# Kernel optimization log

Measured on AMD Instinct MI355X. Metric: run time of the kernel, lower is better.

The kernel has to match this reference:

```python
import jax, jax.numpy as jnp
import numpy as np

A = 3                      # anchors per location
HS = [256, 128, 64, 32]    # square feature-map sizes (FPN levels)
B = 4                      # batch (num images)
SIZES = [A * h * h for h in HS]
T = sum(SIZES)             # 261120 anchors per image
PRE_N, POST_N = 512, 512
NMS_TH, SCORE_TH, MIN_SIZE = 0.7, 0.0, 1e-3
LOG_MAX = 4.135166556742356   # log(1000/16), standard delta clamp
MAXV = 8                      # max vertices of quad-quad intersection
LVL_OFF = 8192.0              # per-level coordinate offset for batched NMS


def box_corners(b):
    # b: [..., 5] (cx, cy, w, h, angle) -> [..., 4, 2] CCW corners
    cx, cy, w, h, a = (b[..., i] for i in range(5))
    c, s = jnp.cos(a), jnp.sin(a)
    dx = 0.5 * jnp.stack([w, -w, -w, w], -1)
    dy = 0.5 * jnp.stack([h, h, -h, -h], -1)
    x = cx[..., None] + dx * c[..., None] - dy * s[..., None]
    y = cy[..., None] + dx * s[..., None] + dy * c[..., None]
    return jnp.stack([x, y], -1)


def _clip(poly, cnt, p1, p2):
    # Sutherland-Hodgman clip of poly (padded [MAXV,2], cnt valid) by half-plane left of p1->p2
    e = p2 - p1
    d = e[0] * (poly[:, 1] - p1[1]) - e[1] * (poly[:, 0] - p1[0])
    def body(carry, i):
        out, oc = carry
        nxt = jnp.where(i + 1 < cnt, i + 1, 0)
        cur_in, nxt_in = d[i] >= 0, d[nxt] >= 0
        valid = i < cnt
        keep = valid & cur_in
        out = out.at[oc].set(jnp.where(keep, poly[i], out[oc]))
        oc = oc + keep.astype(jnp.int32)
        crs = valid & (cur_in != nxt_in)
        den = d[i] - d[nxt]
        t = d[i] / jnp.where(den == 0, 1.0, den)
        ip = poly[i] + t * (poly[nxt] - poly[i])
        out = out.at[oc].set(jnp.where(crs, ip, out[oc]))
        oc = oc + crs.astype(jnp.int32)
        return (out, oc), None
    (out, oc), _ = jax.lax.scan(body, (jnp.zeros((MAXV, 2), poly.dtype), jnp.int32(0)), jnp.arange(MAXV))
    return out, oc


def _inter_area(ca, cb):
    # intersection area of two convex quads given CCW corners [4,2]
    poly = jnp.zeros((MAXV, 2), ca.dtype).at[:4].set(ca)
    cnt = jnp.int32(4)
    for k in range(4):
        poly, cnt = _clip(poly, cnt, cb[k], cb[(k + 1) % 4])
    i = jnp.arange(MAXV)
    nxt = jnp.where(i + 1 < cnt, i + 1, 0)
    cr = poly[i, 0] * poly[nxt, 1] - poly[nxt, 0] * poly[i, 1]
    area = 0.5 * jnp.abs(jnp.sum(jnp.where(i < cnt, cr, 0.0)))
    return jnp.where(cnt >= 3, area, 0.0)


def decode(deltas, anchors):
    # XYWHA decode with 6-dim deltas (dx,dy,dw,dh,dsin,dcos), weights all 1.0
    ax, ay, aw, ah, aa = (anchors[..., i] for i in range(5))
    dx, dy, dw, dh, ds, dc = (deltas[..., i] for i in range(6))
    dw = jnp.minimum(dw, LOG_MAX)
    dh = jnp.minimum(dh, LOG_MAX)
    return jnp.stack([ax + dx * aw, ay + dy * ah, aw * jnp.exp(dw),
                      ah * jnp.exp(dh), aa + jnp.arctan2(ds, dc)], -1)


def nms_image(boxes, scores, levels):
    # boxes [N,5], scores [N] (post-sigmoid), levels [N] int32 -> fixed-size padded outputs
    N = scores.shape[0]
    valid = (boxes[:, 2] >= MIN_SIZE) & (boxes[:, 3] >= MIN_SIZE) & (scores >= SCORE_TH)
    s = jnp.where(valid, scores, -jnp.inf)
    order = jnp.argsort(-s)
    bx, sc, vd = boxes[order], s[order], valid[order]
    off = levels[order].astype(bx.dtype) * LVL_OFF
    nb = bx.at[:, :2].add(off[:, None])          # level offset => cross-level IoU == 0
    nbg = jax.lax.stop_gradient(nb)
    corners = box_corners(nbg)                    # [N,4,2]
    areas = nbg[:, 2] * nbg[:, 3]
    CH = 128
    def chunk_fn(args):
        cc, ca = args
        def row(ci, ai):
            inter = jax.vmap(lambda cj: _inter_area(ci, cj))(corners)
            return inter / (ai + areas - inter + 1e-7)
        return jax.vmap(row)(cc, ca)
    iou = jax.lax.map(chunk_fn, (corners.reshape(N // CH, CH, 4, 2),
                                 areas.reshape(N // CH, CH))).reshape(N, N)
    idx = jnp.arange(N)
    def body(i, sup):
        keep_i = ~sup[i]
        return sup | (keep_i & (iou[i] > NMS_TH) & (idx > i))
    sup = jax.lax.fori_loop(0, N, body, ~vd)      # invalid boxes start suppressed
    kept = ~sup
    _, top_i = jax.lax.top_k(jnp.where(kept, sc, -jnp.inf), POST_N)
    ok = kept[top_i]
    return jnp.where(ok[:, None], bx[top_i], 0.0), jnp.where(ok, sc[top_i], 0.0)


def rpn_forward(objs, dlts, anchors):
    obj_f, dlt_f = [], []
    for o, d, h in zip(objs, dlts, HS):
        # permute_and_flatten: [B,A,H,W] -> [B,H*W*A]; [B,A*6,H,W] -> [B,H*W*A,6]
        obj_f.append(o.transpose(0, 2, 3, 1).reshape(B, -1))
        dlt_f.append(d.reshape(B, A, 6, h, h).transpose(0, 3, 4, 1, 2).reshape(B, -1, 6))
    objectness = jnp.concatenate(obj_f, 1)        # [B, T]
    deltas = jnp.concatenate(dlt_f, 1)            # [B, T, 6]
    proposals = decode(deltas, anchors)           # [B, T, 5]
    parts, offset = [], 0
    for sz in SIZES:                               # per-level top-k
        k = min(PRE_N, sz)
        _, ti = jax.lax.top_k(objectness[:, offset:offset + sz], k)
        parts.append(ti + offset)
        offset += sz
    top_idx = jnp.concatenate(parts, 1)           # [B, 4*PRE_N]
    levels = jnp.concatenate([jnp.full((sz,), i, jnp.int32) for i, sz in enumerate(SIZES)])
    obj_top = jnp.take_along_axis(objectness, top_idx, 1)
    prop_top = jnp.take_along_axis(proposals, top_idx[..., None], 1)
    lvl_top = levels[top_idx]
    scores = jax.nn.sigmoid(obj_top)
    return jax.vmap(nms_image)(prop_top, scores, lvl_top)


def setup_inputs() -> dict:
    key = jax.random.key(0)
    ks = jax.random.split(key, 9)
    inp = {}
    for i, h in enumerate(HS):
        inp[f"obj{i}"] = jax.random.normal(ks[i], (B, A, h, h), jnp.float32)
        inp[f"dlt{i}"] = 0.25 * jax.random.normal(ks[4 + i], (B, A * 6, h, h), jnp.float32)
    u = jax.random.uniform(ks[8], (B, T, 5), jnp.float32)
    inp["anchors"] = jnp.stack([u[..., 0] * 1024.0, u[..., 1] * 1024.0,
                                8.0 + 120.0 * u[..., 2], 8.0 + 120.0 * u[..., 3],
                                jnp.pi * (u[..., 4] - 0.5)], -1)
    return inp


def reference(obj0, obj1, obj2, obj3, dlt0, dlt1, dlt2, dlt3, anchors):
    # returns (boxes [B, POST_N, 5], scores [B, POST_N]) padded with zeros
    return rpn_forward([obj0, obj1, obj2, obj3], [dlt0, dlt1, dlt2, dlt3], anchors)
```

## Files before the change

kernel.cpp:

```cpp
#include <hip/hip_runtime.h>

typedef unsigned int u32;
typedef unsigned long long u64;
typedef unsigned char u8;

#define NB 4
#define T_ANCH 261120
#define NCAND 2048
#define KSEL 512
#define POSTN 512
#define LOG_MAXF 4.135166556742356f
#define NMS_TH 0.7f
#define LVL_OFF_F 8192.0f
#define BINS 4096
#define EQCAP 8192
#define K5_BLOCKS 2048
#define K1_BLOCKS 256

__device__ __forceinline__ u32 mono32(float f){
  u32 u = __float_as_uint(f);
  return (u & 0x80000000u) ? ~u : (u | 0x80000000u);
}
__device__ __forceinline__ int lvl_hw(int lvl){ return 65536 >> (2*lvl); }
__device__ __forceinline__ int lvl_off(int lvl){
  return (lvl>0?196608:0) + (lvl>1?49152:0) + (lvl>2?12288:0);
}
__device__ __forceinline__ void k1_map(int bx, int& b, int& lvl, int& ch){
  b = bx >> 6;
  int c = bx & 63;
  if (c < 48){ lvl = 0; ch = c; }
  else if (c < 60){ lvl = 1; ch = c - 48; }
  else if (c < 63){ lvl = 2; ch = c - 60; }
  else { lvl = 3; ch = 0; }
}

__global__ __launch_bounds__(1024) void k1_hist_thresh(
    const float* __restrict__ o0, const float* __restrict__ o1,
    const float* __restrict__ o2, const float* __restrict__ o3,
    u32* __restrict__ hist16, u32* __restrict__ done16,
    u32* __restrict__ gb0, u32* __restrict__ gcA)
{
  int b, lvl, ch;
  k1_map(blockIdx.x, b, lvl, ch);
  int bid16 = b*4 + lvl;
  int nch = (lvl==0?48 : lvl==1?12 : lvl==2?3 : 1);
  const float* ob = (lvl==0)?o0 : (lvl==1)?o1 : (lvl==2)?o2 : o3;
  int hw = lvl_hw(lvl);
  int size = 3*hw;
  int n4 = size >> 2;
  int i4 = ch*1024 + threadIdx.x;
  __shared__ u32 hist[BINS];
  __shared__ u32 coarse[64];
  __shared__ int s_last;
  for (int i = threadIdx.x; i < BINS; i += 1024) hist[i] = 0;
  __syncthreads();
  if (i4 < n4){
    float4 v = ((const float4*)(ob + (size_t)b*size))[i4];
    atomicAdd(&hist[mono32(v.x) >> 20], 1u);
    atomicAdd(&hist[mono32(v.y) >> 20], 1u);
    atomicAdd(&hist[mono32(v.z) >> 20], 1u);
    atomicAdd(&hist[mono32(v.w) >> 20], 1u);
  }
  __syncthreads();
  u32* gh = hist16 + (size_t)bid16*BINS;
  for (int i = threadIdx.x; i < BINS; i += 1024){
    u32 c = hist[i];
    if (c) atomicAdd(&gh[i], c);
  }
  __syncthreads();
  if (threadIdx.x == 0){
    __threadfence();
    u32 d = atomicAdd(&done16[bid16], 1u);
    s_last = (d == (u32)(nch - 1)) ? 1 : 0;
  }
  __syncthreads();
  if (!s_last) return;

  __threadfence();
  for (int i = threadIdx.x; i < BINS; i += 1024)
    hist[i] = __hip_atomic_load(&gh[i], __ATOMIC_RELAXED, __HIP_MEMORY_SCOPE_AGENT);
  __syncthreads();
  int t = threadIdx.x;
  if (t < 64){
    u32 s = 0;
    for (int z = 0; z < 64; ++z) s += hist[t*64 + z];
    coarse[t] = s;
  }
  __syncthreads();
  if (t == 0){
    u32 acc = 0;
    int cb = 63;
    while (acc + coarse[cb] < (u32)KSEL){ acc += coarse[cb]; --cb; }
    int z = cb*64 + 63;
    while (acc + hist[z] < (u32)KSEL){ acc += hist[z]; --z; }
    gb0[bid16] = (u32)z;
    gcA[bid16] = acc;
  }
}

__global__ __launch_bounds__(1024) void k2_classify(
    const float* __restrict__ o0, const float* __restrict__ o1,
    const float* __restrict__ o2, const float* __restrict__ o3,
    const u32* __restrict__ gb0,
    u32* __restrict__ emitcnt, u32* __restrict__ tiecnt,
    int* __restrict__ cand_j, u64* __restrict__ gtie)
{
  int b, lvl, ch;
  k1_map(blockIdx.x, b, lvl, ch);
  int bid16 = b*4 + lvl;
  const float* ob = (lvl==0)?o0 : (lvl==1)?o1 : (lvl==2)?o2 : o3;
  int hw = lvl_hw(lvl);
  int size = 3*hw;
  int n4 = size >> 2;
  int i4 = ch*1024 + threadIdx.x;

  __shared__ u32 dbuf[KSEL];
  __shared__ u64 tbuf[4096];
  __shared__ u32 dn, tn, dbase, tbase;
  if (threadIdx.x == 0){ dn = 0; tn = 0; }
  __syncthreads();

  u32 b0v = gb0[bid16];
  if (i4 < n4){
    float4 v = ((const float4*)(ob + (size_t)b*size))[i4];
    int L = i4 << 2;
    int a = L / hw;
    int pix = L - a*hw;
    int j0 = pix*3 + a;
    float vv[4] = {v.x, v.y, v.z, v.w};
    #pragma unroll
    for (int q = 0; q < 4; ++q){
      u32 m = mono32(vv[q]);
      u32 bin = m >> 20;
      int j = j0 + 3*q;
      if (bin > b0v){
        u32 s = atomicAdd(&dn, 1u);
        if (s < (u32)KSEL) dbuf[s] = (u32)j;
      } else if (bin == b0v){
        u32 s = atomicAdd(&tn, 1u);
        if (s < 4096u) tbuf[s] = ((u64)m << 32) | (u32)(~(u32)j);
      }
    }
  }
  __syncthreads();
  if (threadIdx.x == 0){
    dbase = dn ? atomicAdd(&emitcnt[bid16], dn) : 0u;
    tbase = tn ? atomicAdd(&tiecnt[bid16], tn) : 0u;
  }
  __syncthreads();
  for (u32 x = threadIdx.x; x < dn; x += 1024){
    u32 s = dbase + x;
    if (s < (u32)KSEL) cand_j[bid16*KSEL + s] = (int)dbuf[x];
  }
  for (u32 x = threadIdx.x; x < tn; x += 1024){
    u32 s = tbase + x;
    if (s < (u32)EQCAP) gtie[(size_t)bid16*EQCAP + s] = tbuf[x];
  }
}

__global__ __launch_bounds__(512) void k3_tie_decode(
    const u64* __restrict__ gtie, const u32* __restrict__ tiecnt,
    const u32* __restrict__ gcA, const int* __restrict__ cand_j,
    const float* __restrict__ o0, const float* __restrict__ o1,
    const float* __restrict__ o2, const float* __restrict__ o3,
    const float* __restrict__ d0, const float* __restrict__ d1,
    const float* __restrict__ d2, const float* __restrict__ d3,
    const float* __restrict__ anchors,
    float* __restrict__ cscore, u32* __restrict__ csmono,
    u64* __restrict__ ctb, float* __restrict__ cbox, u8* __restrict__ cvalid)
{
  int bid = blockIdx.x;
  int t = threadIdx.x;
  __shared__ u64 eq[EQCAP];
  __shared__ u32 wbuf[KSEL];
  __shared__ int jlist[KSEL];
  __shared__ u32 wn;
  u32 n = tiecnt[bid]; if (n > (u32)EQCAP) n = (u32)EQCAP;
  u32 cA = gcA[bid];
  u32 k = (u32)KSEL - cA;
  if (t == 0) wn = 0;
  for (int i = t; i < KSEL; i += 512) jlist[i] = 0;
  for (u32 i = t; i < n; i += 512) eq[i] = gtie[(size_t)bid*EQCAP + i];
  __syncthreads();
  for (u32 i = t; i < n; i += 512){
    u64 ki = eq[i];
    u32 r = 0;
    for (u32 m = 0; m < n; ++m) r += (eq[m] > ki) ? 1u : 0u;
    if (r < k){
      u32 s = atomicAdd(&wn, 1u);
      if (s < (u32)KSEL) wbuf[s] = (u32)(~(u32)ki);
    }
  }
  __syncthreads();
  u32 w = wn;
  for (u32 i = t; i < cA; i += 512)
    if (i < (u32)KSEL) jlist[i] = cand_j[bid*KSEL + i];
  for (u32 x = t; x < w; x += 512){
    u32 s = cA + x;
    if (s < (u32)KSEL) jlist[s] = (int)wbuf[x];
  }
  __syncthreads();

  {
    int c = bid*KSEL + t;
    int b = bid >> 2, lvl = bid & 3;
    int j = jlist[t];
    int hw = lvl_hw(lvl);
    u32 pix = (u32)j / 3u;
    u32 a = (u32)j - pix*3u;
    const float* ob = (lvl==0)?o0 : (lvl==1)?o1 : (lvl==2)?o2 : o3;
    const float* dl = (lvl==0)?d0 : (lvl==1)?d1 : (lvl==2)?d2 : d3;

    float ov = ob[(size_t)(b*3 + (int)a)*hw + pix];
    size_t dbase = ((size_t)(b*3 + (int)a)*6)*(size_t)hw + pix;
    float dx  = dl[dbase + 0*(size_t)hw];
    float dy  = dl[dbase + 1*(size_t)hw];
    float dw  = dl[dbase + 2*(size_t)hw];
    float dh  = dl[dbase + 3*(size_t)hw];
    float dsn = dl[dbase + 4*(size_t)hw];
    float dcs = dl[dbase + 5*(size_t)hw];
    int tt = lvl_off(lvl) + j;
    const float* an = anchors + ((size_t)b*T_ANCH + tt)*5;
    float ax=an[0], ay=an[1], aw=an[2], ah=an[3], aa=an[4];
    dw = fminf(dw, LOG_MAXF); dh = fminf(dh, LOG_MAXF);
    float cx = ax + dx*aw;
    float cy = ay + dy*ah;
    float ww = aw * expf(dw);
    float hh = ah * expf(dh);
    float ang = aa + atan2f(dsn, dcs);
    double sd = 1.0 / (1.0 + exp(-(double)ov));
    float sc = (float)sd;
    bool valid = (ww >= 1e-3f) && (hh >= 1e-3f) && (sc >= 0.0f);
    cscore[c] = sc;
    csmono[c] = valid ? mono32(sc) : 0u;
    ctb[c] = ((u64)lvl << 50) | ((u64)(u32)(~mono32(ov)) << 18) | (u64)(u32)j;
    cvalid[c] = valid ? 1 : 0;
    float* bb = cbox + (size_t)c*5;
    bb[0]=cx; bb[1]=cy; bb[2]=ww; bb[3]=hh; bb[4]=ang;
  }
}

__global__ __launch_bounds__(256) void k4_rank(
    const u32* __restrict__ csmono, const u64* __restrict__ ctb,
    const float* __restrict__ cscore, const float* __restrict__ cbox,
    const u8* __restrict__ cvalid,
    float* __restrict__ sscore, float* __restrict__ sbox,
    float* __restrict__ geom, float4* __restrict__ aabb4,
    u8* __restrict__ svalid, u64* __restrict__ maskz, u64* __restrict__ rowflagz)
{
  int b   = blockIdx.x >> 6;
  int blk = blockIdx.x & 63;
  __shared__ u32 sm[NCAND];
  __shared__ u64 stb[NCAND];
  __shared__ u32 cnt[32][8];
  {
    u64* mz = maskz + (size_t)blockIdx.x * 1024;
    for (int x = threadIdx.x; x < 1024; x += 256) mz[x] = 0ull;
    if (threadIdx.x == 0 && blockIdx.x < NB*32) rowflagz[blockIdx.x] = 0ull;
  }
  for (int k = threadIdx.x; k < NCAND; k += 256){
    sm[k]  = csmono[b*NCAND + k];
    stb[k] = ctb[b*NCAND + k];
  }
  __syncthreads();
  int esub = threadIdx.x >> 3;
  int ssub = threadIdx.x & 7;
  int id = blk*32 + esub;
  u32 ms = sm[id];
  u64 mt = stb[id];
  u32 r = 0;
  #pragma unroll 8
  for (int it = 0; it < 256; ++it){
    int m = it*8 + ssub;
    u32 s2 = sm[m]; u64 t2 = stb[m];
    r += ((s2 > ms) || (s2 == ms && t2 < mt)) ? 1u : 0u;
  }
  cnt[esub][ssub] = r;
  __syncthreads();
  if (ssub == 0){
    u32 rank = 0;
    #pragma unroll
    for (int q = 0; q < 8; ++q) rank += cnt[esub][q];
    int gsrc = b*NCAND + id;
    int gdst = b*NCAND + (int)rank;
    sscore[gdst] = cscore[gsrc];
    svalid[gdst] = cvalid[gsrc];
    float b0 = cbox[(size_t)gsrc*5+0], b1 = cbox[(size_t)gsrc*5+1];
    float b2 = cbox[(size_t)gsrc*5+2], b3 = cbox[(size_t)gsrc*5+3];
    float b4 = cbox[(size_t)gsrc*5+4];
    float* sb = sbox + (size_t)gdst*5;
    sb[0]=b0; sb[1]=b1; sb[2]=b2; sb[3]=b3; sb[4]=b4;
    int lvl = (int)((mt >> 50) & 3ull);
    float offv = (float)lvl * LVL_OFF_F;
    float cx = b0 + offv, cy = b1 + offv, w=b2, h=b3, ang=b4;
    float cc = cosf(ang), sn = sinf(ang);
    float hx = 0.5f*w, hy = 0.5f*h;
    float x0 = cx + hx*cc - hy*sn, y0 = cy + hx*sn + hy*cc;
    float x1 = cx - hx*cc - hy*sn, y1 = cy - hx*sn + hy*cc;
    float x2 = cx - hx*cc + hy*sn, y2 = cy - hx*sn - hy*cc;
    float x3 = cx + hx*cc + hy*sn, y3 = cy + hx*sn - hy*cc;
    float minx = fminf(fminf(x0,x1),fminf(x2,x3));
    float maxx = fmaxf(fmaxf(x0,x1),fmaxf(x2,x3));
    float miny = fminf(fminf(y0,y1),fminf(y2,y3));
    float maxy = fmaxf(fmaxf(y0,y1),fmaxf(y2,y3));
    float* g = geom + (size_t)gdst*16;
    g[0]=minx; g[1]=maxx; g[2]=miny; g[3]=maxy; g[4]=w*h;
    g[5]=x0; g[6]=y0; g[7]=x1; g[8]=y1; g[9]=x2; g[10]=y2; g[11]=x3; g[12]=y3;
    aabb4[gdst] = make_float4(minx, maxx, miny, maxy);
  }
}

__device__ __forceinline__ void emit_pt(float* ox, float* oy, int oc, float x, float y){
  #pragma unroll
  for (int s = 0; s < 8; ++s) if (s == oc){ ox[s] = x; oy[s] = y; }
}

__device__ float quad_inter(const float* ca, const float* cb){
  float px[8], py[8];
  #pragma unroll
  for (int q = 0; q < 8; ++q){ px[q]=0.f; py[q]=0.f; }
  #pragma unroll
  for (int q = 0; q < 4; ++q){ px[q]=ca[2*q]; py[q]=ca[2*q+1]; }
  int cnt = 4;
  #pragma unroll
  for (int e = 0; e < 4; ++e){
    float p1x = cb[2*e],         p1y = cb[2*e+1];
    float p2x = cb[(2*e+2)&7],   p2y = cb[(2*e+3)&7];
    float ex = p2x-p1x, ey = p2y-p1y;
    float d[8];
    #pragma unroll
    for (int q = 0; q < 8; ++q) d[q] = ex*(py[q]-p1y) - ey*(px[q]-p1x);
    float ox[8], oy[8];
    #pragma unroll
    for (int q = 0; q < 8; ++q){ ox[q]=0.f; oy[q]=0.f; }
    int oc = 0;
    #pragma unroll
    for (int q = 0; q < 8; ++q){
      if (q < cnt){
        bool last = (q+1 >= cnt);
        float dn  = last ? d[0]  : d[(q+1)&7];
        bool in0 = (d[q] >= 0.0f), in1 = (dn >= 0.0f);
        if (in0){ emit_pt(ox,oy,oc,px[q],py[q]); oc++; }
        if (in0 != in1){
          float pnx = last ? px[0] : px[(q+1)&7];
          float pny = last ? py[0] : py[(q+1)&7];
          float den = d[q] - dn;
          float t = d[q] / ((den == 0.0f) ? 1.0f : den);
          emit_pt(ox,oy,oc, px[q] + t*(pnx-px[q]), py[q] + t*(pny-py[q]));
          oc++;
        }
      }
    }
    cnt = (oc > 8) ? 8 : oc;
    #pragma unroll
    for (int q = 0; q < 8; ++q){ px[q]=ox[q]; py[q]=oy[q]; }
  }
  if (cnt < 3) return 0.0f;
  float s = 0.0f;
  #pragma unroll
  for (int q = 0; q < 8; ++q){
    if (q < cnt){
      bool last = (q+1 >= cnt);
      float pnx = last ? px[0] : px[(q+1)&7];
      float pny = last ? py[0] : py[(q+1)&7];
      s += px[q]*pny - pnx*py[q];
    }
  }
  return 0.5f*fabsf(s);
}

__global__ __launch_bounds__(256) void k5_pairs(
    const float4* __restrict__ aabb4, const float* __restrict__ geom,
    u64* __restrict__ mask, u64* __restrict__ rowflag)
{
  __shared__ u32 lbuf[4096];
  __shared__ u32 lcnt;
  if (threadIdx.x == 0) lcnt = 0;
  __syncthreads();
  int img = blockIdx.x >> 9;
  int kk  = blockIdx.x & 511;
  int lane = threadIdx.x & 63;
  int rows[4] = {2*kk, 2*kk + 1, 2046 - 2*kk, 2047 - 2*kk};
  #pragma unroll
  for (int r = 0; r < 4; ++r){
    int i = rows[r];
    float4 gi = aabb4[img*NCAND + i];
    for (int j = i + 1 + (int)threadIdx.x; j < NCAND; j += 256){
      float4 gj = aabb4[img*NCAND + j];
      bool pass = !(gi.x > gj.y || gj.x > gi.y || gi.z > gj.w || gj.z > gi.w);
      u64 bm = __ballot(pass);
      if (bm){
        int leader = __ffsll((long long)bm) - 1;
        u32 base = 0;
        if (lane == leader) base = atomicAdd(&lcnt, (u32)__popcll(bm));
        base = (u32)__shfl((int)base, leader);
        if (pass){
          u32 off = (u32)__popcll(bm & ((1ull << lane) - 1ull));
          lbuf[base + off] = (u32)((i << 11) | j);
        }
      }
    }
  }
  __syncthreads();
  u32 n = lcnt;
  for (u32 x = threadIdx.x; x < n; x += 256){
    u32 gt = lbuf[x];
    int i = (int)(gt >> 11);
    int j = (int)(gt & (NCAND-1));
    const float* gi = geom + ((size_t)(img*NCAND + i))*16;
    const float* gj = geom + ((size_t)(img*NCAND + j))*16;
    float inter = quad_inter(gi+5, gj+5);
    float iou = inter / (gi[4] + gj[4] - inter + 1e-7f);
    if (iou > NMS_TH){
      atomicOr(&mask[((size_t)(img*NCAND + i))*32 + (j >> 6)], 1ull << (j & 63));
      atomicOr(&rowflag[(size_t)img*32 + (i >> 6)], 1ull << (i & 63));
    }
  }
}

__global__ __launch_bounds__(1024) void k6_nms_out(
    const u64* __restrict__ mask, const u64* __restrict__ rowflag,
    const u8* __restrict__ svalid,
    const float* __restrict__ sbox, const float* __restrict__ sscore,
    float* __restrict__ out)
{
  int b = blockIdx.x;
  __shared__ u32 fid[NCAND];
  __shared__ u32 wcnt[32], wpref[32];
  __shared__ u64 s_kept[32];
  __shared__ u32 pref[32];
  __shared__ u32 s_F;
  int t = threadIdx.x;
  int wid = t >> 6, lane = t & 63;

  if (t < 32) wcnt[t] = (u32)__popcll(rowflag[b*32 + t]);
  __syncthreads();
  if (t == 0){
    u32 run = 0;
    for (int w = 0; w < 32; ++w){ wpref[w] = run; run += wcnt[w]; }
    s_F = run;
  }
  __syncthreads();
  if (t < 32){
    u64 fw = rowflag[b*32 + t];
    u32 o = wpref[t];
    while (fw){
      int bpos = __builtin_ctzll(fw);
      fid[o++] = (u32)(t*64 + bpos);
      fw &= fw - 1;
    }
  }
  for (int x = t; x < POSTN*5; x += 1024) out[(size_t)b*POSTN*5 + x] = 0.0f;
  for (int x = t; x < POSTN;   x += 1024) out[(size_t)NB*POSTN*5 + b*POSTN + x] = 0.0f;
  __syncthreads();

  if (wid == 0){
    u32 slo = 0, shi = 0;
    {
      int wl = lane & 31;
      u64 w = 0;
      for (int q = 0; q < 64; ++q)
        if (!svalid[b*NCAND + wl*64 + q]) w |= (1ull << q);
      slo = (u32)w; shi = (u32)(w >> 32);
    }
    u32 F = s_F;
    const u64* mb = mask + ((size_t)b*NCAND)*32;
    for (u32 f = 0; f < F; f += 8){
      u32 myfid = 0;
      if (f + (lane & 7) < F) myfid = fid[f + (lane & 7)];
      u64 v[8];
      #pragma unroll
      for (int q = 0; q < 8; ++q){
        if (f + q < F){
          u32 fq = (u32)__builtin_amdgcn_readlane((int)myfid, q);
          v[q] = mb[(size_t)fq*32 + (lane & 31)];
        } else v[q] = 0ull;
      }
      #pragma unroll
      for (int q = 0; q < 8; ++q){
        if (f + q < F){
          u32 i = (u32)__builtin_amdgcn_readlane((int)myfid, q);
          int wi = (int)(i >> 6);
          u32 wlo = (u32)__builtin_amdgcn_readlane((int)slo, wi);
          u32 whi = (u32)__builtin_amdgcn_readlane((int)shi, wi);
          u64 w = ((u64)whi << 32) | wlo;
          u32 keep = (u32)((~w >> (i & 63)) & 1ull);
          u64 vm = v[q] & (0ull - (u64)keep);
          slo |= (u32)vm; shi |= (u32)(vm >> 32);
        }
      }
    }
    if (lane < 32) s_kept[lane] = ~(((u64)shi << 32) | slo);
  }
  __syncthreads();

  if (t < 32) pref[t] = (u32)__popcll(s_kept[t]);
  __syncthreads();
  if (t == 0){
    u32 run = 0;
    for (int w = 0; w < 32; ++w){ u32 tv = pref[w]; pref[w] = run; run += tv; }
  }
  __syncthreads();
  for (int i = t; i < NCAND; i += 1024){
    u64 kw = s_kept[i >> 6];
    if ((kw >> (i & 63)) & 1ull){
      u32 rank = pref[i >> 6] + (u32)__popcll(kw & ((1ull << (i & 63)) - 1ull));
      if (rank < POSTN){
        const float* bp = sbox + ((size_t)(b*NCAND + i))*5;
        float* op = out + ((size_t)(b*POSTN + rank))*5;
        op[0]=bp[0]; op[1]=bp[1]; op[2]=bp[2]; op[3]=bp[3]; op[4]=bp[4];
        out[(size_t)NB*POSTN*5 + b*POSTN + rank] = sscore[b*NCAND + i];
      }
    }
  }
}

extern "C" void kernel_launch(void* const* d_in, const int* in_sizes, int n_in,
                              void* d_out, int out_size, void* d_ws, size_t ws_size,
                              hipStream_t stream)
{
  (void)out_size; (void)ws_size;
  const float *obj[4] = {nullptr,nullptr,nullptr,nullptr};
  const float *dlt[4] = {nullptr,nullptr,nullptr,nullptr};
  const float *anchors = nullptr;
  for (int i = 0; i < n_in; ++i){
    int s = in_sizes[i];
    const float* p = (const float*)d_in[i];
    switch (s){
      case 786432:  obj[0] = p; break;
      case 4718592: dlt[0] = p; break;
      case 196608:  obj[1] = p; break;
      case 1179648: dlt[1] = p; break;
      case 49152:   obj[2] = p; break;
      case 294912:  dlt[2] = p; break;
      case 12288:   obj[3] = p; break;
      case 73728:   dlt[3] = p; break;
      case 5222400: anchors = p; break;
      default: break;
    }
  }

  char* wsb = (char*)d_ws;
  size_t off = 0;
  auto alloc = [&](size_t bytes)->void*{
    size_t cur = (off + 255) & ~(size_t)255;
    off = cur + bytes;
    return (void*)(wsb + cur);
  };
  int*   cand_j = (int*)  alloc(16*KSEL*sizeof(int));
  float* cscore = (float*)alloc((size_t)NB*NCAND*sizeof(float));
  u32*   csmono = (u32*)  alloc((size_t)NB*NCAND*sizeof(u32));
  u64*   ctb    = (u64*)  alloc((size_t)NB*NCAND*sizeof(u64));
  float* cbox   = (float*)alloc((size_t)NB*NCAND*5*sizeof(float));
  u8*    cvalid = (u8*)   alloc((size_t)NB*NCAND);
  float* sscore = (float*)alloc((size_t)NB*NCAND*sizeof(float));
  float* sbox   = (float*)alloc((size_t)NB*NCAND*5*sizeof(float));
  u8*    svalid = (u8*)   alloc((size_t)NB*NCAND);
  float* geom   = (float*)alloc((size_t)NB*NCAND*16*sizeof(float));
  float4* aabb4 = (float4*)alloc((size_t)NB*NCAND*sizeof(float4));
  u64*   gtie   = (u64*)  alloc((size_t)16*EQCAP*sizeof(u64));
  u64*   maskp  = (u64*)  alloc((size_t)NB*NCAND*32*sizeof(u64));
  u64*   rowflag= (u64*)  alloc((size_t)NB*32*sizeof(u64));
  u32*   gb0    = (u32*)  alloc(16*sizeof(u32));
  u32*   gcA    = (u32*)  alloc(16*sizeof(u32));
  u32*   hist16 = (u32*)  alloc((size_t)16*BINS*sizeof(u32));
  u32*   done16 = (u32*)  alloc(16*sizeof(u32));
  u32*   emitc  = (u32*)  alloc(16*sizeof(u32));
  u32*   tiec   = (u32*)  alloc(16*sizeof(u32));
  size_t zero_len = (size_t)((wsb + off) - (char*)hist16);

  hipMemsetAsync(hist16, 0, zero_len, stream);

  hipLaunchKernelGGL(k1_hist_thresh, dim3(K1_BLOCKS), dim3(1024), 0, stream,
                     obj[0], obj[1], obj[2], obj[3], hist16, done16, gb0, gcA);
  hipLaunchKernelGGL(k2_classify, dim3(K1_BLOCKS), dim3(1024), 0, stream,
                     obj[0], obj[1], obj[2], obj[3], gb0, emitc, tiec,
                     cand_j, gtie);
  hipLaunchKernelGGL(k3_tie_decode, dim3(16), dim3(512), 0, stream,
                     gtie, tiec, gcA, cand_j,
                     obj[0], obj[1], obj[2], obj[3],
                     dlt[0], dlt[1], dlt[2], dlt[3],
                     anchors, cscore, csmono, ctb, cbox, cvalid);
  hipLaunchKernelGGL(k4_rank, dim3(256), dim3(256), 0, stream,
                     csmono, ctb, cscore, cbox, cvalid, sscore, sbox, geom,
                     aabb4, svalid, maskp, rowflag);
  hipLaunchKernelGGL(k5_pairs, dim3(K5_BLOCKS), dim3(256), 0, stream,
                     aabb4, geom, maskp, rowflag);
  hipLaunchKernelGGL(k6_nms_out, dim3(4), dim3(1024), 0, stream,
                     maskp, rowflag, svalid, sbox, sscore, (float*)d_out);
}
```

Measured before the change: 192.3 us.

## Fuse all RPN stages into one cooperative persistent kernel with grid syncs

Replaces the memset and six separate kernel launches with a single cooperative kernel of 256 blocks of 1024 threads. Stages are separated by grid-wide barriers, and a shared-memory union is reused across stages. Zeroing of the workspace and output is folded into the first stage. The aim is to remove launch gaps and the memset, but stages that used many smaller blocks (pair tests, ranking) now run on a fixed grid with grid-sync overhead, and the large shared union may limit occupancy.

```diff
diff --git a/kernel.cpp b/kernel.cpp
--- a/kernel.cpp
+++ b/kernel.cpp
@@ -1,4 +1,7 @@
 #include <hip/hip_runtime.h>
+#include <hip/hip_cooperative_groups.h>
+
+namespace cg = cooperative_groups;
 
 typedef unsigned int u32;
 typedef unsigned long long u64;
@@ -14,8 +17,7 @@
 #define LVL_OFF_F 8192.0f
 #define BINS 4096
 #define EQCAP 8192
-#define K5_BLOCKS 2048
-#define K1_BLOCKS 256
+#define GRID 256
 
 __device__ __forceinline__ u32 mono32(float f){
   u32 u = __float_as_uint(f);
@@ -32,282 +34,6 @@
   else if (c < 60){ lvl = 1; ch = c - 48; }
   else if (c < 63){ lvl = 2; ch = c - 60; }
   else { lvl = 3; ch = 0; }
-}
-
-__global__ __launch_bounds__(1024) void k1_hist_thresh(
-    const float* __restrict__ o0, const float* __restrict__ o1,
-    const float* __restrict__ o2, const float* __restrict__ o3,
-    u32* __restrict__ hist16, u32* __restrict__ done16,
-    u32* __restrict__ gb0, u32* __restrict__ gcA)
-{
-  int b, lvl, ch;
-  k1_map(blockIdx.x, b, lvl, ch);
-  int bid16 = b*4 + lvl;
-  int nch = (lvl==0?48 : lvl==1?12 : lvl==2?3 : 1);
-  const float* ob = (lvl==0)?o0 : (lvl==1)?o1 : (lvl==2)?o2 : o3;
-  int hw = lvl_hw(lvl);
-  int size = 3*hw;
-  int n4 = size >> 2;
-  int i4 = ch*1024 + threadIdx.x;
-  __shared__ u32 hist[BINS];
-  __shared__ u32 coarse[64];
-  __shared__ int s_last;
-  for (int i = threadIdx.x; i < BINS; i += 1024) hist[i] = 0;
-  __syncthreads();
-  if (i4 < n4){
-    float4 v = ((const float4*)(ob + (size_t)b*size))[i4];
-    atomicAdd(&hist[mono32(v.x) >> 20], 1u);
-    atomicAdd(&hist[mono32(v.y) >> 20], 1u);
-    atomicAdd(&hist[mono32(v.z) >> 20], 1u);
-    atomicAdd(&hist[mono32(v.w) >> 20], 1u);
-  }
-  __syncthreads();
-  u32* gh = hist16 + (size_t)bid16*BINS;
-  for (int i = threadIdx.x; i < BINS; i += 1024){
-    u32 c = hist[i];
-    if (c) atomicAdd(&gh[i], c);
-  }
-  __syncthreads();
-  if (threadIdx.x == 0){
-    __threadfence();
-    u32 d = atomicAdd(&done16[bid16], 1u);
-    s_last = (d == (u32)(nch - 1)) ? 1 : 0;
-  }
-  __syncthreads();
-  if (!s_last) return;
-
-  __threadfence();
-  for (int i = threadIdx.x; i < BINS; i += 1024)
-    hist[i] = __hip_atomic_load(&gh[i], __ATOMIC_RELAXED, __HIP_MEMORY_SCOPE_AGENT);
-  __syncthreads();
-  int t = threadIdx.x;
-  if (t < 64){
-    u32 s = 0;
-    for (int z = 0; z < 64; ++z) s += hist[t*64 + z];
-    coarse[t] = s;
-  }
-  __syncthreads();
-  if (t == 0){
-    u32 acc = 0;
-    int cb = 63;
-    while (acc + coarse[cb] < (u32)KSEL){ acc += coarse[cb]; --cb; }
-    int z = cb*64 + 63;
-    while (acc + hist[z] < (u32)KSEL){ acc += hist[z]; --z; }
-    gb0[bid16] = (u32)z;
-    gcA[bid16] = acc;
-  }
-}
-
-__global__ __launch_bounds__(1024) void k2_classify(
-    const float* __restrict__ o0, const float* __restrict__ o1,
-    const float* __restrict__ o2, const float* __restrict__ o3,
-    const u32* __restrict__ gb0,
-    u32* __restrict__ emitcnt, u32* __restrict__ tiecnt,
-    int* __restrict__ cand_j, u64* __restrict__ gtie)
-{
-  int b, lvl, ch;
-  k1_map(blockIdx.x, b, lvl, ch);
-  int bid16 = b*4 + lvl;
-  const float* ob = (lvl==0)?o0 : (lvl==1)?o1 : (lvl==2)?o2 : o3;
-  int hw = lvl_hw(lvl);
-  int size = 3*hw;
-  int n4 = size >> 2;
-  int i4 = ch*1024 + threadIdx.x;
-
-  __shared__ u32 dbuf[KSEL];
-  __shared__ u64 tbuf[4096];
-  __shared__ u32 dn, tn, dbase, tbase;
-  if (threadIdx.x == 0){ dn = 0; tn = 0; }
-  __syncthreads();
-
-  u32 b0v = gb0[bid16];
-  if (i4 < n4){
-    float4 v = ((const float4*)(ob + (size_t)b*size))[i4];
-    int L = i4 << 2;
-    int a = L / hw;
-    int pix = L - a*hw;
-    int j0 = pix*3 + a;
-    float vv[4] = {v.x, v.y, v.z, v.w};
-    #pragma unroll
-    for (int q = 0; q < 4; ++q){
-      u32 m = mono32(vv[q]);
-      u32 bin = m >> 20;
-      int j = j0 + 3*q;
-      if (bin > b0v){
-        u32 s = atomicAdd(&dn, 1u);
-        if (s < (u32)KSEL) dbuf[s] = (u32)j;
-      } else if (bin == b0v){
-        u32 s = atomicAdd(&tn, 1u);
-        if (s < 4096u) tbuf[s] = ((u64)m << 32) | (u32)(~(u32)j);
-      }
-    }
-  }
-  __syncthreads();
-  if (threadIdx.x == 0){
-    dbase = dn ? atomicAdd(&emitcnt[bid16], dn) : 0u;
-    tbase = tn ? atomicAdd(&tiecnt[bid16], tn) : 0u;
-  }
-  __syncthreads();
-  for (u32 x = threadIdx.x; x < dn; x += 1024){
-    u32 s = dbase + x;
-    if (s < (u32)KSEL) cand_j[bid16*KSEL + s] = (int)dbuf[x];
-  }
-  for (u32 x = threadIdx.x; x < tn; x += 1024){
-    u32 s = tbase + x;
-    if (s < (u32)EQCAP) gtie[(size_t)bid16*EQCAP + s] = tbuf[x];
-  }
-}
-
-__global__ __launch_bounds__(512) void k3_tie_decode(
-    const u64* __restrict__ gtie, const u32* __restrict__ tiecnt,
-    const u32* __restrict__ gcA, const int* __restrict__ cand_j,
-    const float* __restrict__ o0, const float* __restrict__ o1,
-    const float* __restrict__ o2, const float* __restrict__ o3,
-    const float* __restrict__ d0, const float* __restrict__ d1,
-    const float* __restrict__ d2, const float* __restrict__ d3,
-    const float* __restrict__ anchors,
-    float* __restrict__ cscore, u32* __restrict__ csmono,
-    u64* __restrict__ ctb, float* __restrict__ cbox, u8* __restrict__ cvalid)
-{
-  int bid = blockIdx.x;
-  int t = threadIdx.x;
-  __shared__ u64 eq[EQCAP];
-  __shared__ u32 wbuf[KSEL];
-  __shared__ int jlist[KSEL];
-  __shared__ u32 wn;
-  u32 n = tiecnt[bid]; if (n > (u32)EQCAP) n = (u32)EQCAP;
-  u32 cA = gcA[bid];
-  u32 k = (u32)KSEL - cA;
-  if (t == 0) wn = 0;
-  for (int i = t; i < KSEL; i += 512) jlist[i] = 0;
-  for (u32 i = t; i < n; i += 512) eq[i] = gtie[(size_t)bid*EQCAP + i];
-  __syncthreads();
-  for (u32 i = t; i < n; i += 512){
-    u64 ki = eq[i];
-    u32 r = 0;
-    for (u32 m = 0; m < n; ++m) r += (eq[m] > ki) ? 1u : 0u;
-    if (r < k){
-      u32 s = atomicAdd(&wn, 1u);
-      if (s < (u32)KSEL) wbuf[s] = (u32)(~(u32)ki);
-    }
-  }
-  __syncthreads();
-  u32 w = wn;
-  for (u32 i = t; i < cA; i += 512)
-    if (i < (u32)KSEL) jlist[i] = cand_j[bid*KSEL + i];
-  for (u32 x = t; x < w; x += 512){
-    u32 s = cA + x;
-    if (s < (u32)KSEL) jlist[s] = (int)wbuf[x];
-  }
-  __syncthreads();
-
-  {
-    int c = bid*KSEL + t;
-    int b = bid >> 2, lvl = bid & 3;
-    int j = jlist[t];
-    int hw = lvl_hw(lvl);
-    u32 pix = (u32)j / 3u;
-    u32 a = (u32)j - pix*3u;
-    const float* ob = (lvl==0)?o0 : (lvl==1)?o1 : (lvl==2)?o2 : o3;
-    const float* dl = (lvl==0)?d0 : (lvl==1)?d1 : (lvl==2)?d2 : d3;
-
-    float ov = ob[(size_t)(b*3 + (int)a)*hw + pix];
-    size_t dbase = ((size_t)(b*3 + (int)a)*6)*(size_t)hw + pix;
-    float dx  = dl[dbase + 0*(size_t)hw];
-    float dy  = dl[dbase + 1*(size_t)hw];
-    float dw  = dl[dbase + 2*(size_t)hw];
-    float dh  = dl[dbase + 3*(size_t)hw];
-    float dsn = dl[dbase + 4*(size_t)hw];
-    float dcs = dl[dbase + 5*(size_t)hw];
-    int tt = lvl_off(lvl) + j;
-    const float* an = anchors + ((size_t)b*T_ANCH + tt)*5;
-    float ax=an[0], ay=an[1], aw=an[2], ah=an[3], aa=an[4];
-    dw = fminf(dw, LOG_MAXF); dh = fminf(dh, LOG_MAXF);
-    float cx = ax + dx*aw;
-    float cy = ay + dy*ah;
-    float ww = aw * expf(dw);
-    float hh = ah * expf(dh);
-    float ang = aa + atan2f(dsn, dcs);
-    double sd = 1.0 / (1.0 + exp(-(double)ov));
-    float sc = (float)sd;
-    bool valid = (ww >= 1e-3f) && (hh >= 1e-3f) && (sc >= 0.0f);
-    cscore[c] = sc;
-    csmono[c] = valid ? mono32(sc) : 0u;
-    ctb[c] = ((u64)lvl << 50) | ((u64)(u32)(~mono32(ov)) << 18) | (u64)(u32)j;
-    cvalid[c] = valid ? 1 : 0;
-    float* bb = cbox + (size_t)c*5;
-    bb[0]=cx; bb[1]=cy; bb[2]=ww; bb[3]=hh; bb[4]=ang;
-  }
-}
-
-__global__ __launch_bounds__(256) void k4_rank(
-    const u32* __restrict__ csmono, const u64* __restrict__ ctb,
-    const float* __restrict__ cscore, const float* __restrict__ cbox,
-    const u8* __restrict__ cvalid,
-    float* __restrict__ sscore, float* __restrict__ sbox,
-    float* __restrict__ geom, float4* __restrict__ aabb4,
-    u8* __restrict__ svalid, u64* __restrict__ maskz, u64* __restrict__ rowflagz)
-{
-  int b   = blockIdx.x >> 6;
-  int blk = blockIdx.x & 63;
-  __shared__ u32 sm[NCAND];
-  __shared__ u64 stb[NCAND];
-  __shared__ u32 cnt[32][8];
-  {
-    u64* mz = maskz + (size_t)blockIdx.x * 1024;
-    for (int x = threadIdx.x; x < 1024; x += 256) mz[x] = 0ull;
-    if (threadIdx.x == 0 && blockIdx.x < NB*32) rowflagz[blockIdx.x] = 0ull;
-  }
-  for (int k = threadIdx.x; k < NCAND; k += 256){
-    sm[k]  = csmono[b*NCAND + k];
-    stb[k] = ctb[b*NCAND + k];
-  }
-  __syncthreads();
-  int esub = threadIdx.x >> 3;
-  int ssub = threadIdx.x & 7;
-  int id = blk*32 + esub;
-  u32 ms = sm[id];
-  u64 mt = stb[id];
-  u32 r = 0;
-  #pragma unroll 8
-  for (int it = 0; it < 256; ++it){
-    int m = it*8 + ssub;
-    u32 s2 = sm[m]; u64 t2 = stb[m];
-    r += ((s2 > ms) || (s2 == ms && t2 < mt)) ? 1u : 0u;
-  }
-  cnt[esub][ssub] = r;
-  __syncthreads();
-  if (ssub == 0){
-    u32 rank = 0;
-    #pragma unroll
-    for (int q = 0; q < 8; ++q) rank += cnt[esub][q];
-    int gsrc = b*NCAND + id;
-    int gdst = b*NCAND + (int)rank;
-    sscore[gdst] = cscore[gsrc];
-    svalid[gdst] = cvalid[gsrc];
-    float b0 = cbox[(size_t)gsrc*5+0], b1 = cbox[(size_t)gsrc*5+1];
-    float b2 = cbox[(size_t)gsrc*5+2], b3 = cbox[(size_t)gsrc*5+3];
-    float b4 = cbox[(size_t)gsrc*5+4];
-    float* sb = sbox + (size_t)gdst*5;
-    sb[0]=b0; sb[1]=b1; sb[2]=b2; sb[3]=b3; sb[4]=b4;
-    int lvl = (int)((mt >> 50) & 3ull);
-    float offv = (float)lvl * LVL_OFF_F;
-    float cx = b0 + offv, cy = b1 + offv, w=b2, h=b3, ang=b4;
-    float cc = cosf(ang), sn = sinf(ang);
-    float hx = 0.5f*w, hy = 0.5f*h;
-    float x0 = cx + hx*cc - hy*sn, y0 = cy + hx*sn + hy*cc;
-    float x1 = cx - hx*cc - hy*sn, y1 = cy - hx*sn + hy*cc;
-    float x2 = cx - hx*cc + hy*sn, y2 = cy - hx*sn - hy*cc;
-    float x3 = cx + hx*cc + hy*sn, y3 = cy + hx*sn - hy*cc;
-    float minx = fminf(fminf(x0,x1),fminf(x2,x3));
-    float maxx = fmaxf(fmaxf(x0,x1),fmaxf(x2,x3));
-    float miny = fminf(fminf(y0,y1),fminf(y2,y3));
-    float maxy = fmaxf(fmaxf(y0,y1),fmaxf(y2,y3));
-    float* g = geom + (size_t)gdst*16;
-    g[0]=minx; g[1]=maxx; g[2]=miny; g[3]=maxy; g[4]=w*h;
-    g[5]=x0; g[6]=y0; g[7]=x1; g[8]=y1; g[9]=x2; g[10]=y2; g[11]=x3; g[12]=y3;
-    aabb4[gdst] = make_float4(minx, maxx, miny, maxy);
-  }
 }
 
 __device__ __forceinline__ void emit_pt(float* ox, float* oy, int oc, float x, float y){
@@ -369,147 +95,397 @@
   return 0.5f*fabsf(s);
 }
 
-__global__ __launch_bounds__(256) void k5_pairs(
-    const float4* __restrict__ aabb4, const float* __restrict__ geom,
-    u64* __restrict__ mask, u64* __restrict__ rowflag)
+struct MegaArgs {
+  const float *o0,*o1,*o2,*o3;
+  const float *d0,*d1,*d2,*d3;
+  const float *anchors;
+  u32 *hist16, *gb0, *gcA, *emitc, *tiec;
+  u64 *gtie;
+  int *cand_j;
+  float *cscore; u32 *csmono; u64 *ctb; float *cbox; u8 *cvalid;
+  float *sscore, *sbox; u8 *svalid; float *geom; float4 *aabb4;
+  u64 *maskp, *rowflag;
+  float *out;
+};
+
+union SharedU {
+  struct { u32 hist[BINS]; u32 coarse[64]; } p1;
+  struct { u32 dbuf[KSEL]; u64 tbuf[4096]; u32 dn,tn,dbase,tbase; } p2;
+  struct { u64 eq[EQCAP]; u32 wbuf[KSEL]; int jlist[KSEL]; u32 wn; } p3;
+  struct { u32 sm[NCAND]; u64 stb[NCAND]; u32 cnt[32][32]; } p4;
+  struct { u32 lbuf[4096]; u32 lcnt; } p5;
+  struct { u32 fid[NCAND]; u32 wcnt[32], wpref[32];
+           u64 s_kept[32]; u32 pref[32]; u32 sF; } p6;
+};
+
+__global__ __launch_bounds__(1024) void mega(MegaArgs A)
 {
-  __shared__ u32 lbuf[4096];
-  __shared__ u32 lcnt;
-  if (threadIdx.x == 0) lcnt = 0;
-  __syncthreads();
-  int img = blockIdx.x >> 9;
-  int kk  = blockIdx.x & 511;
-  int lane = threadIdx.x & 63;
-  int rows[4] = {2*kk, 2*kk + 1, 2046 - 2*kk, 2047 - 2*kk};
-  #pragma unroll
-  for (int r = 0; r < 4; ++r){
-    int i = rows[r];
-    float4 gi = aabb4[img*NCAND + i];
-    for (int j = i + 1 + (int)threadIdx.x; j < NCAND; j += 256){
-      float4 gj = aabb4[img*NCAND + j];
-      bool pass = !(gi.x > gj.y || gj.x > gi.y || gi.z > gj.w || gj.z > gi.w);
-      u64 bm = __ballot(pass);
-      if (bm){
-        int leader = __ffsll((long long)bm) - 1;
-        u32 base = 0;
-        if (lane == leader) base = atomicAdd(&lcnt, (u32)__popcll(bm));
-        base = (u32)__shfl((int)base, leader);
-        if (pass){
-          u32 off = (u32)__popcll(bm & ((1ull << lane) - 1ull));
-          lbuf[base + off] = (u32)((i << 11) | j);
-        }
-      }
-    }
-  }
-  __syncthreads();
-  u32 n = lcnt;
-  for (u32 x = threadIdx.x; x < n; x += 256){
-    u32 gt = lbuf[x];
-    int i = (int)(gt >> 11);
-    int j = (int)(gt & (NCAND-1));
-    const float* gi = geom + ((size_t)(img*NCAND + i))*16;
-    const float* gj = geom + ((size_t)(img*NCAND + j))*16;
-    float inter = quad_inter(gi+5, gj+5);
-    float iou = inter / (gi[4] + gj[4] - inter + 1e-7f);
-    if (iou > NMS_TH){
-      atomicOr(&mask[((size_t)(img*NCAND + i))*32 + (j >> 6)], 1ull << (j & 63));
-      atomicOr(&rowflag[(size_t)img*32 + (i >> 6)], 1ull << (i & 63));
-    }
-  }
-}
-
-__global__ __launch_bounds__(1024) void k6_nms_out(
-    const u64* __restrict__ mask, const u64* __restrict__ rowflag,
-    const u8* __restrict__ svalid,
-    const float* __restrict__ sbox, const float* __restrict__ sscore,
-    float* __restrict__ out)
-{
-  int b = blockIdx.x;
-  __shared__ u32 fid[NCAND];
-  __shared__ u32 wcnt[32], wpref[32];
-  __shared__ u64 s_kept[32];
-  __shared__ u32 pref[32];
-  __shared__ u32 s_F;
-  int t = threadIdx.x;
-  int wid = t >> 6, lane = t & 63;
-
-  if (t < 32) wcnt[t] = (u32)__popcll(rowflag[b*32 + t]);
-  __syncthreads();
-  if (t == 0){
-    u32 run = 0;
-    for (int w = 0; w < 32; ++w){ wpref[w] = run; run += wcnt[w]; }
-    s_F = run;
-  }
-  __syncthreads();
-  if (t < 32){
-    u64 fw = rowflag[b*32 + t];
-    u32 o = wpref[t];
-    while (fw){
-      int bpos = __builtin_ctzll(fw);
-      fid[o++] = (u32)(t*64 + bpos);
-      fw &= fw - 1;
-    }
-  }
-  for (int x = t; x < POSTN*5; x += 1024) out[(size_t)b*POSTN*5 + x] = 0.0f;
-  for (int x = t; x < POSTN;   x += 1024) out[(size_t)NB*POSTN*5 + b*POSTN + x] = 0.0f;
-  __syncthreads();
-
-  if (wid == 0){
-    u32 slo = 0, shi = 0;
-    {
-      int wl = lane & 31;
-      u64 w = 0;
-      for (int q = 0; q < 64; ++q)
-        if (!svalid[b*NCAND + wl*64 + q]) w |= (1ull << q);
-      slo = (u32)w; shi = (u32)(w >> 32);
-    }
-    u32 F = s_F;
-    const u64* mb = mask + ((size_t)b*NCAND)*32;
-    for (u32 f = 0; f < F; f += 8){
-      u32 myfid = 0;
-      if (f + (lane & 7) < F) myfid = fid[f + (lane & 7)];
-      u64 v[8];
+  cg::grid_group grid = cg::this_grid();
+  __shared__ SharedU sh;
+  const int t = threadIdx.x;
+  const int bx = blockIdx.x;
+  const u64 gtid = (u64)bx*1024 + t;
+
+  {
+    A.maskp[gtid] = 0ull;
+    if (gtid < (u64)16*BINS) A.hist16[gtid] = 0u;
+    if (gtid < NB*32) A.rowflag[gtid] = 0ull;
+    if (gtid < 16){ A.emitc[gtid] = 0u; A.tiec[gtid] = 0u; }
+    if (gtid < (u64)NB*POSTN*6) A.out[gtid] = 0.0f;
+  }
+  grid.sync();
+
+  {
+    int b, lvl, ch;
+    k1_map(bx, b, lvl, ch);
+    int bid16 = b*4 + lvl;
+    const float* ob = (lvl==0)?A.o0 : (lvl==1)?A.o1 : (lvl==2)?A.o2 : A.o3;
+    int hw = lvl_hw(lvl);
+    int size = 3*hw;
+    int n4 = size >> 2;
+    int i4 = ch*1024 + t;
+    for (int i = t; i < BINS; i += 1024) sh.p1.hist[i] = 0;
+    __syncthreads();
+    if (i4 < n4){
+      float4 v = ((const float4*)(ob + (size_t)b*size))[i4];
+      atomicAdd(&sh.p1.hist[mono32(v.x) >> 20], 1u);
+      atomicAdd(&sh.p1.hist[mono32(v.y) >> 20], 1u);
+      atomicAdd(&sh.p1.hist[mono32(v.z) >> 20], 1u);
+      atomicAdd(&sh.p1.hist[mono32(v.w) >> 20], 1u);
+    }
+    __syncthreads();
+    u32* gh = A.hist16 + (size_t)bid16*BINS;
+    for (int i = t; i < BINS; i += 1024){
+      u32 c = sh.p1.hist[i];
+      if (c) atomicAdd(&gh[i], c);
+    }
+  }
+  grid.sync();
+
+  if (bx < 16){
+    const u32* gh = A.hist16 + (size_t)bx*BINS;
+    for (int i = t; i < BINS; i += 1024) sh.p1.hist[i] = gh[i];
+    __syncthreads();
+    if (t < 64){
+      u32 s = 0;
+      for (int z = 0; z < 64; ++z) s += sh.p1.hist[t*64 + z];
+      sh.p1.coarse[t] = s;
+    }
+    __syncthreads();
+    if (t == 0){
+      u32 acc = 0;
+      int cb = 63;
+      while (acc + sh.p1.coarse[cb] < (u32)KSEL){ acc += sh.p1.coarse[cb]; --cb; }
+      int z = cb*64 + 63;
+      while (acc + sh.p1.hist[z] < (u32)KSEL){ acc += sh.p1.hist[z]; --z; }
+      A.gb0[bx] = (u32)z;
+      A.gcA[bx] = acc;
+    }
+  }
+  grid.sync();
+
+  {
+    int b, lvl, ch;
+    k1_map(bx, b, lvl, ch);
+    int bid16 = b*4 + lvl;
+    const float* ob = (lvl==0)?A.o0 : (lvl==1)?A.o1 : (lvl==2)?A.o2 : A.o3;
+    int hw = lvl_hw(lvl);
+    int size = 3*hw;
+    int n4 = size >> 2;
+    int i4 = ch*1024 + t;
+    if (t == 0){ sh.p2.dn = 0; sh.p2.tn = 0; }
+    __syncthreads();
+    u32 b0v = A.gb0[bid16];
+    if (i4 < n4){
+      float4 v = ((const float4*)(ob + (size_t)b*size))[i4];
+      int L = i4 << 2;
+      int a = L / hw;
+      int pix = L - a*hw;
+      int j0 = pix*3 + a;
+      float vv[4] = {v.x, v.y, v.z, v.w};
       #pragma unroll
-      for (int q = 0; q < 8; ++q){
-        if (f + q < F){
-          u32 fq = (u32)__builtin_amdgcn_readlane((int)myfid, q);
-          v[q] = mb[(size_t)fq*32 + (lane & 31)];
-        } else v[q] = 0ull;
-      }
+      for (int q = 0; q < 4; ++q){
+        u32 m = mono32(vv[q]);
+        u32 bin = m >> 20;
+        int j = j0 + 3*q;
+        if (bin > b0v){
+          u32 s = atomicAdd(&sh.p2.dn, 1u);
+          if (s < (u32)KSEL) sh.p2.dbuf[s] = (u32)j;
+        } else if (bin == b0v){
+          u32 s = atomicAdd(&sh.p2.tn, 1u);
+          if (s < 4096u) sh.p2.tbuf[s] = ((u64)m << 32) | (u32)(~(u32)j);
+        }
+      }
+    }
+    __syncthreads();
+    if (t == 0){
+      sh.p2.dbase = sh.p2.dn ? atomicAdd(&A.emitc[bid16], sh.p2.dn) : 0u;
+      sh.p2.tbase = sh.p2.tn ? atomicAdd(&A.tiec[bid16], sh.p2.tn) : 0u;
+    }
+    __syncthreads();
+    for (u32 x = t; x < sh.p2.dn; x += 1024){
+      u32 s = sh.p2.dbase + x;
+      if (s < (u32)KSEL) A.cand_j[bid16*KSEL + s] = (int)sh.p2.dbuf[x];
+    }
+    for (u32 x = t; x < sh.p2.tn; x += 1024){
+      u32 s = sh.p2.tbase + x;
+      if (s < (u32)EQCAP) A.gtie[(size_t)bid16*EQCAP + s] = sh.p2.tbuf[x];
+    }
+  }
+  grid.sync();
+
+  if (bx < 16){
+    int bid = bx;
+    u32 n = A.tiec[bid]; if (n > (u32)EQCAP) n = (u32)EQCAP;
+    u32 cA = A.gcA[bid];
+    u32 k = (u32)KSEL - cA;
+    if (t == 0) sh.p3.wn = 0;
+    for (int i = t; i < KSEL; i += 1024) sh.p3.jlist[i] = 0;
+    for (u32 i = t; i < n; i += 1024) sh.p3.eq[i] = A.gtie[(size_t)bid*EQCAP + i];
+    __syncthreads();
+    for (u32 i = t; i < n; i += 1024){
+      u64 ki = sh.p3.eq[i];
+      u32 r = 0;
+      for (u32 m = 0; m < n; ++m) r += (sh.p3.eq[m] > ki) ? 1u : 0u;
+      if (r < k){
+        u32 s = atomicAdd(&sh.p3.wn, 1u);
+        if (s < (u32)KSEL) sh.p3.wbuf[s] = (u32)(~(u32)ki);
+      }
+    }
+    __syncthreads();
+    u32 w = sh.p3.wn; if (w > (u32)KSEL) w = (u32)KSEL;
+    for (u32 i = t; i < cA; i += 1024)
+      if (i < (u32)KSEL) sh.p3.jlist[i] = A.cand_j[bid*KSEL + i];
+    for (u32 x = t; x < w; x += 1024){
+      u32 s = cA + x;
+      if (s < (u32)KSEL) sh.p3.jlist[s] = (int)sh.p3.wbuf[x];
+    }
+    __syncthreads();
+
+    if (t < KSEL){
+      int c = bid*KSEL + t;
+      int b = bid >> 2, lvl = bid & 3;
+      int j = sh.p3.jlist[t];
+      int hw = lvl_hw(lvl);
+      u32 pix = (u32)j / 3u;
+      u32 a = (u32)j - pix*3u;
+      const float* ob = (lvl==0)?A.o0 : (lvl==1)?A.o1 : (lvl==2)?A.o2 : A.o3;
+      const float* dl = (lvl==0)?A.d0 : (lvl==1)?A.d1 : (lvl==2)?A.d2 : A.d3;
+
+      float ov = ob[(size_t)(b*3 + (int)a)*hw + pix];
+      size_t dbase = ((size_t)(b*3 + (int)a)*6)*(size_t)hw + pix;
+      float dx  = dl[dbase + 0*(size_t)hw];
+      float dy  = dl[dbase + 1*(size_t)hw];
+      float dw  = dl[dbase + 2*(size_t)hw];
+      float dh  = dl[dbase + 3*(size_t)hw];
+      float dsn = dl[dbase + 4*(size_t)hw];
+      float dcs = dl[dbase + 5*(size_t)hw];
+      int tt = lvl_off(lvl) + j;
+      const float* an = A.anchors + ((size_t)b*T_ANCH + tt)*5;
+      float ax=an[0], ay=an[1], aw=an[2], ah=an[3], aa=an[4];
+      dw = fminf(dw, LOG_MAXF); dh = fminf(dh, LOG_MAXF);
+      float cx = ax + dx*aw;
+      float cy = ay + dy*ah;
+      float ww = aw * expf(dw);
+      float hh = ah * expf(dh);
+      float ang = aa + atan2f(dsn, dcs);
+      double sd = 1.0 / (1.0 + exp(-(double)ov));
+      float sc = (float)sd;
+      bool valid = (ww >= 1e-3f) && (hh >= 1e-3f) && (sc >= 0.0f);
+      A.cscore[c] = sc;
+      A.csmono[c] = valid ? mono32(sc) : 0u;
+      A.ctb[c] = ((u64)lvl << 50) | ((u64)(u32)(~mono32(ov)) << 18) | (u64)(u32)j;
+      A.cvalid[c] = valid ? 1 : 0;
+      float* bb = A.cbox + (size_t)c*5;
+      bb[0]=cx; bb[1]=cy; bb[2]=ww; bb[3]=hh; bb[4]=ang;
+    }
+  }
+  grid.sync();
+
+  {
+    int b   = bx >> 6;
+    int blk = bx & 63;
+    for (int k2 = t; k2 < NCAND; k2 += 1024){
+      sh.p4.sm[k2]  = A.csmono[b*NCAND + k2];
+      sh.p4.stb[k2] = A.ctb[b*NCAND + k2];
+    }
+    __syncthreads();
+    int esub = t >> 5;
+    int ssub = t & 31;
+    int id = blk*32 + esub;
+    u32 ms = sh.p4.sm[id];
+    u64 mt = sh.p4.stb[id];
+    u32 r = 0;
+    #pragma unroll 8
+    for (int it = 0; it < 64; ++it){
+      int m = it*32 + ssub;
+      u32 s2 = sh.p4.sm[m]; u64 t2 = sh.p4.stb[m];
+      r += ((s2 > ms) || (s2 == ms && t2 < mt)) ? 1u : 0u;
+    }
+    sh.p4.cnt[esub][ssub] = r;
+    __syncthreads();
+    if (ssub == 0){
+      u32 rank = 0;
       #pragma unroll
-      for (int q = 0; q < 8; ++q){
-        if (f + q < F){
-          u32 i = (u32)__builtin_amdgcn_readlane((int)myfid, q);
-          int wi = (int)(i >> 6);
-          u32 wlo = (u32)__builtin_amdgcn_readlane((int)slo, wi);
-          u32 whi = (u32)__builtin_amdgcn_readlane((int)shi, wi);
-          u64 w = ((u64)whi << 32) | wlo;
-          u32 keep = (u32)((~w >> (i & 63)) & 1ull);
-          u64 vm = v[q] & (0ull - (u64)keep);
-          slo |= (u32)vm; shi |= (u32)(vm >> 32);
-        }
-      }
-    }
-    if (lane < 32) s_kept[lane] = ~(((u64)shi << 32) | slo);
-  }
-  __syncthreads();
-
-  if (t < 32) pref[t] = (u32)__popcll(s_kept[t]);
-  __syncthreads();
-  if (t == 0){
-    u32 run = 0;
-    for (int w = 0; w < 32; ++w){ u32 tv = pref[w]; pref[w] = run; run += tv; }
-  }
-  __syncthreads();
-  for (int i = t; i < NCAND; i += 1024){
-    u64 kw = s_kept[i >> 6];
-    if ((kw >> (i & 63)) & 1ull){
-      u32 rank = pref[i >> 6] + (u32)__popcll(kw & ((1ull << (i & 63)) - 1ull));
-      if (rank < POSTN){
-        const float* bp = sbox + ((size_t)(b*NCAND + i))*5;
-        float* op = out + ((size_t)(b*POSTN + rank))*5;
-        op[0]=bp[0]; op[1]=bp[1]; op[2]=bp[2]; op[3]=bp[3]; op[4]=bp[4];
-        out[(size_t)NB*POSTN*5 + b*POSTN + rank] = sscore[b*NCAND + i];
+      for (int q = 0; q < 32; ++q) rank += sh.p4.cnt[esub][q];
+      int gsrc = b*NCAND + id;
+      int gdst = b*NCAND + (int)rank;
+      A.sscore[gdst] = A.cscore[gsrc];
+      A.svalid[gdst] = A.cvalid[gsrc];
+      float b0 = A.cbox[(size_t)gsrc*5+0], b1 = A.cbox[(size_t)gsrc*5+1];
+      float b2 = A.cbox[(size_t)gsrc*5+2], b3 = A.cbox[(size_t)gsrc*5+3];
+      float b4 = A.cbox[(size_t)gsrc*5+4];
+      float* sb = A.sbox + (size_t)gdst*5;
+      sb[0]=b0; sb[1]=b1; sb[2]=b2; sb[3]=b3; sb[4]=b4;
+      int lvl = (int)((mt >> 50) & 3ull);
+      float offv = (float)lvl * LVL_OFF_F;
+      float cx = b0 + offv, cy = b1 + offv, w=b2, h=b3, ang=b4;
+      float cc = cosf(ang), sn = sinf(ang);
+      float hx = 0.5f*w, hy = 0.5f*h;
+      float x0 = cx + hx*cc - hy*sn, y0 = cy + hx*sn + hy*cc;
+      float x1 = cx - hx*cc - hy*sn, y1 = cy - hx*sn + hy*cc;
+      float x2 = cx - hx*cc + hy*sn, y2 = cy - hx*sn - hy*cc;
+      float x3 = cx + hx*cc + hy*sn, y3 = cy + hx*sn - hy*cc;
+      float minx = fminf(fminf(x0,x1),fminf(x2,x3));
+      float maxx = fmaxf(fmaxf(x0,x1),fmaxf(x2,x3));
+      float miny = fminf(fminf(y0,y1),fminf(y2,y3));
+      float maxy = fmaxf(fmaxf(y0,y1),fmaxf(y2,y3));
+      float* g = A.geom + (size_t)gdst*16;
+      g[0]=minx; g[1]=maxx; g[2]=miny; g[3]=maxy; g[4]=w*h;
+      g[5]=x0; g[6]=y0; g[7]=x1; g[8]=y1; g[9]=x2; g[10]=y2; g[11]=x3; g[12]=y3;
+      A.aabb4[gdst] = make_float4(minx, maxx, miny, maxy);
+    }
+  }
+  grid.sync();
+
+  {
+    int lane = t & 63;
+    for (int task = bx; task < 2048; task += GRID){
+      int img = task >> 9;
+      int kk  = task & 511;
+      __syncthreads();
+      if (t == 0) sh.p5.lcnt = 0;
+      __syncthreads();
+      int rows[4] = {2*kk, 2*kk + 1, 2046 - 2*kk, 2047 - 2*kk};
+      #pragma unroll
+      for (int r = 0; r < 4; ++r){
+        int i = rows[r];
+        float4 gi = A.aabb4[img*NCAND + i];
+        for (int j = i + 1 + t; j < NCAND; j += 1024){
+          float4 gj = A.aabb4[img*NCAND + j];
+          bool pass = !(gi.x > gj.y || gj.x > gi.y || gi.z > gj.w || gj.z > gi.w);
+          u64 bm = __ballot(pass);
+          if (bm){
+            int leader = __ffsll((long long)bm) - 1;
+            u32 base = 0;
+            if (lane == leader) base = atomicAdd(&sh.p5.lcnt, (u32)__popcll(bm));
+            base = (u32)__shfl((int)base, leader);
+            if (pass){
+              u32 off = (u32)__popcll(bm & ((1ull << lane) - 1ull));
+              sh.p5.lbuf[base + off] = (u32)((i << 11) | j);
+            }
+          }
+        }
+      }
+      __syncthreads();
+      u32 n = sh.p5.lcnt;
+      for (u32 x = t; x < n; x += 1024){
+        u32 gt = sh.p5.lbuf[x];
+        int i = (int)(gt >> 11);
+        int j = (int)(gt & (NCAND-1));
+        const float* gi = A.geom + ((size_t)(img*NCAND + i))*16;
+        const float* gj = A.geom + ((size_t)(img*NCAND + j))*16;
+        float inter = quad_inter(gi+5, gj+5);
+        float iou = inter / (gi[4] + gj[4] - inter + 1e-7f);
+        if (iou > NMS_TH){
+          atomicOr(&A.maskp[((size_t)(img*NCAND + i))*32 + (j >> 6)], 1ull << (j & 63));
+          atomicOr(&A.rowflag[(size_t)img*32 + (i >> 6)], 1ull << (i & 63));
+        }
+      }
+    }
+  }
+  grid.sync();
+
+  if (bx < NB){
+    int b = bx;
+    int wid = t >> 6, lane = t & 63;
+
+    if (t < 32) sh.p6.wcnt[t] = (u32)__popcll(A.rowflag[b*32 + t]);
+    __syncthreads();
+    if (t == 0){
+      u32 run = 0;
+      for (int w = 0; w < 32; ++w){ sh.p6.wpref[w] = run; run += sh.p6.wcnt[w]; }
+      sh.p6.sF = run;
+    }
+    __syncthreads();
+    if (t < 32){
+      u64 fw = A.rowflag[b*32 + t];
+      u32 o = sh.p6.wpref[t];
+      while (fw){
+        int bpos = __builtin_ctzll(fw);
+        sh.p6.fid[o++] = (u32)(t*64 + bpos);
+        fw &= fw - 1;
+      }
+    }
+    __syncthreads();
+
+    if (wid == 0){
+      u32 slo = 0, shi = 0;
+      {
+        int wl = lane & 31;
+        u64 w = 0;
+        for (int q = 0; q < 64; ++q)
+          if (!A.svalid[b*NCAND + wl*64 + q]) w |= (1ull << q);
+        slo = (u32)w; shi = (u32)(w >> 32);
+      }
+      u32 F = sh.p6.sF;
+      const u64* mb = A.maskp + ((size_t)b*NCAND)*32;
+      for (u32 f = 0; f < F; f += 8){
+        u32 myfid = 0;
+        if (f + (lane & 7) < F) myfid = sh.p6.fid[f + (lane & 7)];
+        u64 v[8];
+        #pragma unroll
+        for (int q = 0; q < 8; ++q){
+          if (f + q < F){
+            u32 fq = (u32)__builtin_amdgcn_readlane((int)myfid, q);
+            v[q] = mb[(size_t)fq*32 + (lane & 31)];
+          } else v[q] = 0ull;
+        }
+        #pragma unroll
+        for (int q = 0; q < 8; ++q){
+          if (f + q < F){
+            u32 i = (u32)__builtin_amdgcn_readlane((int)myfid, q);
+            int wi = (int)(i >> 6);
+            u32 wlo = (u32)__builtin_amdgcn_readlane((int)slo, wi);
+            u32 whi = (u32)__builtin_amdgcn_readlane((int)shi, wi);
+            u64 w = ((u64)whi << 32) | wlo;
+            u32 keep = (u32)((~w >> (i & 63)) & 1ull);
+            u64 vm = v[q] & (0ull - (u64)keep);
+            slo |= (u32)vm; shi |= (u32)(vm >> 32);
+          }
+        }
+      }
+      if (lane < 32) sh.p6.s_kept[lane] = ~(((u64)shi << 32) | slo);
+    }
+    __syncthreads();
+
+    if (t < 32) sh.p6.pref[t] = (u32)__popcll(sh.p6.s_kept[t]);
+    __syncthreads();
+    if (t == 0){
+      u32 run = 0;
+      for (int w = 0; w < 32; ++w){ u32 tv = sh.p6.pref[w]; sh.p6.pref[w] = run; run += tv; }
+    }
+    __syncthreads();
+    for (int i = t; i < NCAND; i += 1024){
+      u64 kw = sh.p6.s_kept[i >> 6];
+      if ((kw >> (i & 63)) & 1ull){
+        u32 rank = sh.p6.pref[i >> 6] + (u32)__popcll(kw & ((1ull << (i & 63)) - 1ull));
+        if (rank < POSTN){
+          const float* bp = A.sbox + ((size_t)(b*NCAND + i))*5;
+          float* op = A.out + ((size_t)(b*POSTN + rank))*5;
+          op[0]=bp[0]; op[1]=bp[1]; op[2]=bp[2]; op[3]=bp[3]; op[4]=bp[4];
+          A.out[(size_t)NB*POSTN*5 + b*POSTN + rank] = A.sscore[b*NCAND + i];
+        }
       }
     }
   }
@@ -547,45 +523,32 @@
     off = cur + bytes;
     return (void*)(wsb + cur);
   };
-  int*   cand_j = (int*)  alloc(16*KSEL*sizeof(int));
-  float* cscore = (float*)alloc((size_t)NB*NCAND*sizeof(float));
-  u32*   csmono = (u32*)  alloc((size_t)NB*NCAND*sizeof(u32));
-  u64*   ctb    = (u64*)  alloc((size_t)NB*NCAND*sizeof(u64));
-  float* cbox   = (float*)alloc((size_t)NB*NCAND*5*sizeof(float));
-  u8*    cvalid = (u8*)   alloc((size_t)NB*NCAND);
-  float* sscore = (float*)alloc((size_t)NB*NCAND*sizeof(float));
-  float* sbox   = (float*)alloc((size_t)NB*NCAND*5*sizeof(float));
-  u8*    svalid = (u8*)   alloc((size_t)NB*NCAND);
-  float* geom   = (float*)alloc((size_t)NB*NCAND*16*sizeof(float));
-  float4* aabb4 = (float4*)alloc((size_t)NB*NCAND*sizeof(float4));
-  u64*   gtie   = (u64*)  alloc((size_t)16*EQCAP*sizeof(u64));
-  u64*   maskp  = (u64*)  alloc((size_t)NB*NCAND*32*sizeof(u64));
-  u64*   rowflag= (u64*)  alloc((size_t)NB*32*sizeof(u64));
-  u32*   gb0    = (u32*)  alloc(16*sizeof(u32));
-  u32*   gcA    = (u32*)  alloc(16*sizeof(u32));
-  u32*   hist16 = (u32*)  alloc((size_t)16*BINS*sizeof(u32));
-  u32*   done16 = (u32*)  alloc(16*sizeof(u32));
-  u32*   emitc  = (u32*)  alloc(16*sizeof(u32));
-  u32*   tiec   = (u32*)  alloc(16*sizeof(u32));
-  size_t zero_len = (size_t)((wsb + off) - (char*)hist16);
-
-  hipMemsetAsync(hist16, 0, zero_len, stream);
-
-  hipLaunchKernelGGL(k1_hist_thresh, dim3(K1_BLOCKS), dim3(1024), 0, stream,
-                     obj[0], obj[1], obj[2], obj[3], hist16, done16, gb0, gcA);
-  hipLaunchKernelGGL(k2_classify, dim3(K1_BLOCKS), dim3(1024), 0, stream,
-                     obj[0], obj[1], obj[2], obj[3], gb0, emitc, tiec,
-                     cand_j, gtie);
-  hipLaunchKernelGGL(k3_tie_decode, dim3(16), dim3(512), 0, stream,
-                     gtie, tiec, gcA, cand_j,
-                     obj[0], obj[1], obj[2], obj[3],
-                     dlt[0], dlt[1], dlt[2], dlt[3],
-                     anchors, cscore, csmono, ctb, cbox, cvalid);
-  hipLaunchKernelGGL(k4_rank, dim3(256), dim3(256), 0, stream,
-                     csmono, ctb, cscore, cbox, cvalid, sscore, sbox, geom,
-                     aabb4, svalid, maskp, rowflag);
-  hipLaunchKernelGGL(k5_pairs, dim3(K5_BLOCKS), dim3(256), 0, stream,
-                     aabb4, geom, maskp, rowflag);
-  hipLaunchKernelGGL(k6_nms_out, dim3(4), dim3(1024), 0, stream,
-                     maskp, rowflag, svalid, sbox, sscore, (float*)d_out);
-}
+  MegaArgs A;
+  A.o0 = obj[0]; A.o1 = obj[1]; A.o2 = obj[2]; A.o3 = obj[3];
+  A.d0 = dlt[0]; A.d1 = dlt[1]; A.d2 = dlt[2]; A.d3 = dlt[3];
+  A.anchors = anchors;
+  A.cand_j = (int*)  alloc(16*KSEL*sizeof(int));
+  A.cscore = (float*)alloc((size_t)NB*NCAND*sizeof(float));
+  A.csmono = (u32*)  alloc((size_t)NB*NCAND*sizeof(u32));
+  A.ctb    = (u64*)  alloc((size_t)NB*NCAND*sizeof(u64));
+  A.cbox   = (float*)alloc((size_t)NB*NCAND*5*sizeof(float));
+  A.cvalid = (u8*)   alloc((size_t)NB*NCAND);
+  A.sscore = (float*)alloc((size_t)NB*NCAND*sizeof(float));
+  A.sbox   = (float*)alloc((size_t)NB*NCAND*5*sizeof(float));
+  A.svalid = (u8*)   alloc((size_t)NB*NCAND);
+  A.geom   = (float*)alloc((size_t)NB*NCAND*16*sizeof(float));
+  A.aabb4  = (float4*)alloc((size_t)NB*NCAND*sizeof(float4));
+  A.gtie   = (u64*)  alloc((size_t)16*EQCAP*sizeof(u64));
+  A.maskp  = (u64*)  alloc((size_t)NB*NCAND*32*sizeof(u64));
+  A.rowflag= (u64*)  alloc((size_t)NB*32*sizeof(u64));
+  A.hist16 = (u32*)  alloc((size_t)16*BINS*sizeof(u32));
+  A.gb0    = (u32*)  alloc(16*sizeof(u32));
+  A.gcA    = (u32*)  alloc(16*sizeof(u32));
+  A.emitc  = (u32*)  alloc(16*sizeof(u32));
+  A.tiec   = (u32*)  alloc(16*sizeof(u32));
+  A.out    = (float*)d_out;
+
+  void* kargs[] = { (void*)&A };
+  hipLaunchCooperativeKernel((const void*)mega, dim3(GRID), dim3(1024),
+                             kargs, 0, stream);
+}
```

Result: slower. 404.9 us (+110.6%).
